# Optimization experiments

Hardware: AMD Instinct MI355X
Metric: run time of the kernel (lower is better)

The kernel has to match this reference:

```python
import jax, jax.numpy as jnp
import numpy as np

SIGMA = 1.0

def setup_inputs() -> dict:
    key = jax.random.key(0)
    k1, k2 = jax.random.split(key)
    z = jax.random.normal(k1, (8192, 1024), dtype=jnp.float32)
    expert_keys = jax.random.normal(k2, (4096, 1024), dtype=jnp.float32)
    return {"z": z, "expert_keys": expert_keys}

def reference(z, expert_keys):
    # squared euclidean distances [N, E] = |z|^2 + |e|^2 - 2 z.e
    z_sq = jnp.sum(z * z, axis=-1, keepdims=True)          # [N, 1]
    e_sq = jnp.sum(expert_keys * expert_keys, axis=-1)     # [E]
    dist2 = z_sq + e_sq[None, :] - 2.0 * (z @ expert_keys.T)
    dist2 = jnp.maximum(dist2, 0.0)
    similarity = jnp.exp(-dist2 / (2.0 * SIGMA ** 2))       # [N, E]
    weights = jax.nn.softmax(similarity, axis=-1)            # [N, E]
    weighted_expert = weights @ expert_keys                  # [N, D]
    return (similarity, weighted_expert)
```

## Files before the change

kernel.cpp:

```cpp
#include <hip/hip_runtime.h>
#include <stdint.h>


#define M_TOK 8192
#define N_EXP 4096
#define D_DIM 1024

typedef __attribute__((ext_vector_type(4))) float f32x4;
typedef __attribute__((ext_vector_type(8))) short short8;
typedef __attribute__((ext_vector_type(4))) unsigned short u16x4;
typedef unsigned short u16;
typedef unsigned int u32;

__device__ __forceinline__ u16 f32_to_bf16(float f) {
  u32 u = __builtin_bit_cast(u32, f);
  u += 0x7fff + ((u >> 16) & 1);
  return (u16)(u >> 16);
}

__device__ __forceinline__ void async16(const void* g, void* l) {
  __builtin_amdgcn_global_load_lds((__attribute__((address_space(1))) void*)(g),
                                   (__attribute__((address_space(3))) void*)(l),
                                   16, 0, 0);
}

__global__ __launch_bounds__(256) void prep_convert2(const float* __restrict__ zsrc,
                                                     const float* __restrict__ esrc,
                                                     u16* __restrict__ zdst,
                                                     u16* __restrict__ edst,
                                                     float* __restrict__ zsq,
                                                     float* __restrict__ esq) {
  int row = blockIdx.x;
  const float* src;
  u16* dst;
  float* sq;
  if (row < M_TOK) {
    src = zsrc + (size_t)row * D_DIM;
    dst = zdst + (size_t)row * D_DIM;
    sq = zsq + row;
  } else {
    int r = row - M_TOK;
    src = esrc + (size_t)r * D_DIM;
    dst = edst + (size_t)r * D_DIM;
    sq = esq + r;
  }
  int t = threadIdx.x;
  const float4 v = ((const float4*)src)[t];
  ushort4 h;
  h.x = f32_to_bf16(v.x); h.y = f32_to_bf16(v.y);
  h.z = f32_to_bf16(v.z); h.w = f32_to_bf16(v.w);
  ((ushort4*)dst)[t] = h;
  float p = v.x * v.x + v.y * v.y + v.z * v.z + v.w * v.w;
#pragma unroll
  for (int off = 1; off < 64; off <<= 1) p += __shfl_xor(p, off, 64);
  __shared__ float partial[4];
  if ((t & 63) == 0) partial[t >> 6] = p;
  __syncthreads();
  if (t == 0) *sq = partial[0] + partial[1] + partial[2] + partial[3];
}

__global__ __launch_bounds__(256) void transpose_bf16(const u16* __restrict__ src,
                                                      u16* __restrict__ dst) {
  __shared__ u16 tile[64][65];
  int e0 = blockIdx.x * 64;
  int d0 = blockIdx.y * 64;
  int t = threadIdx.x;
  int lr = t >> 4;
  int lc = (t & 15) * 4;
#pragma unroll
  for (int r8 = 0; r8 < 4; ++r8) {
    int row = lr + r8 * 16;
    ushort4 v = *(const ushort4*)(src + (size_t)(e0 + row) * D_DIM + d0 + lc);
    tile[row][lc + 0] = v.x; tile[row][lc + 1] = v.y;
    tile[row][lc + 2] = v.z; tile[row][lc + 3] = v.w;
  }
  __syncthreads();
#pragma unroll
  for (int r8 = 0; r8 < 4; ++r8) {
    int dl = lr + r8 * 16;
    ushort4 v;
    v.x = tile[lc + 0][dl]; v.y = tile[lc + 1][dl];
    v.z = tile[lc + 2][dl]; v.w = tile[lc + 3][dl];
    *(ushort4*)(dst + (size_t)(d0 + dl) * N_EXP + e0 + lc) = v;
  }
}

template <int EPI>
__global__ __launch_bounds__(512, 4) void gemm_bt(const u16* __restrict__ A,
                                                  const u16* __restrict__ Bt,
                                                  int Mdim, int Ndim, int Kdim,
                                                  float* __restrict__ out, int ldo,
                                                  const float* __restrict__ a_sq,
                                                  const float* __restrict__ b_sq,
                                                  float* __restrict__ rowsum,
                                                  u16* __restrict__ wb,
                                                  const float* __restrict__ scale) {
  constexpr int BM = 128, BN = 128, BK = 64;
  __shared__ __align__(16) u16 smA[2 * BM * BK];
  __shared__ __align__(16) u16 smB[2 * BN * BK];

  const int nTilesN = Ndim / BN;
  const int nwg = (Mdim / BM) * nTilesN;
  const int cpx = nwg >> 3;
  const int wg = blockIdx.x;
  const int swz = (wg & 7) * cpx + (wg >> 3);
  const int m0 = (swz / nTilesN) * BM;
  const int n0 = (swz % nTilesN) * BN;

  const int t = threadIdx.x;
  const int l = t & 63;
  const int w = t >> 6;
  const int wr = w >> 2;
  const int wc = w & 3;
  const int lr8 = l >> 3;
  const int cswz = (((l & 7) ^ lr8) << 3);
  const int s0 = w * 2, s1 = w * 2 + 1;
  const int str0 = s0 * 8 + lr8, str1 = s1 * 8 + lr8;

  f32x4 acc[4][2];
#pragma unroll
  for (int i = 0; i < 4; ++i)
#pragma unroll
    for (int j = 0; j < 2; ++j) acc[i][j] = (f32x4){0.f, 0.f, 0.f, 0.f};

  const int nIter = Kdim / BK;
  async16(A + (size_t)(m0 + str0) * Kdim + cswz, smA + s0 * 512);
  async16(A + (size_t)(m0 + str1) * Kdim + cswz, smA + s1 * 512);
  async16(Bt + (size_t)(n0 + str0) * Kdim + cswz, smB + s0 * 512);
  async16(Bt + (size_t)(n0 + str1) * Kdim + cswz, smB + s1 * 512);
  __syncthreads();

  int cur = 0;
  for (int it = 0; it < nIter; ++it) {
    if (it + 1 < nIter) {
      const int k0 = (it + 1) * BK;
      const int nb = (cur ^ 1) * 8192;
      async16(A + (size_t)(m0 + str0) * Kdim + k0 + cswz, smA + nb + s0 * 512);
      async16(A + (size_t)(m0 + str1) * Kdim + k0 + cswz, smA + nb + s1 * 512);
      async16(Bt + (size_t)(n0 + str0) * Kdim + k0 + cswz, smB + nb + s0 * 512);
      async16(Bt + (size_t)(n0 + str1) * Kdim + k0 + cswz, smB + nb + s1 * 512);
    }
    const int cbase = cur * 8192;
#pragma unroll
    for (int ks = 0; ks < 2; ++ks) {
      short8 af[4], bf[2];
      const int lrow = l & 15;
      const int kb = ks * 64 + ((l >> 4) << 4);
#pragma unroll
      for (int mi = 0; mi < 4; ++mi) {
        int row = wr * 64 + mi * 16 + lrow;
        int addr = row * 128 + (kb ^ ((row & 7) << 4));
        af[mi] = *(const short8*)(smA + cbase + (addr >> 1));
      }
#pragma unroll
      for (int ni = 0; ni < 2; ++ni) {
        int row = wc * 32 + ni * 16 + lrow;
        int addr = row * 128 + (kb ^ ((row & 7) << 4));
        bf[ni] = *(const short8*)(smB + cbase + (addr >> 1));
      }
#pragma unroll
      for (int mi = 0; mi < 4; ++mi)
#pragma unroll
        for (int ni = 0; ni < 2; ++ni)
          acc[mi][ni] = __builtin_amdgcn_mfma_f32_16x16x32_bf16(
              bf[ni], af[mi], acc[mi][ni], 0, 0, 0);
    }
    __syncthreads();
    cur ^= 1;
  }

  const int lcol = l & 15;
  const int rgrp = l >> 4;
  if (EPI == 1) {
    float* ldsT = ((float*)smA) + w * (16 * 36);
    const int rr = l >> 3;
    const int c4 = (l & 7) * 4;
#pragma unroll
    for (int mi = 0; mi < 4; ++mi) {
      int grow = m0 + wr * 64 + mi * 16 + lcol;
      float zq = a_sq[grow];
#pragma unroll
      for (int ni = 0; ni < 2; ++ni) {
        int ncol = n0 + wc * 32 + ni * 16 + rgrp * 4;
        f32x4 eqv = *(const f32x4*)(b_sq + ncol);
        f32x4 simv;
#pragma unroll
        for (int r = 0; r < 4; ++r) {
          float dist2 = fmaxf(zq + eqv[r] - 2.0f * acc[mi][ni][r], 0.0f);
          simv[r] = __expf(-0.5f * dist2);
        }
        *(f32x4*)(ldsT + lcol * 36 + ni * 16 + rgrp * 4) = simv;
      }
      asm volatile("s_waitcnt lgkmcnt(0)" ::: "memory");
#pragma unroll
      for (int pass = 0; pass < 2; ++pass) {
        int rrow = pass * 8 + rr;
        f32x4 sv = *(const f32x4*)(ldsT + rrow * 36 + c4);
        int growr = m0 + wr * 64 + mi * 16 + rrow;
        size_t gbase = (size_t)growr * ldo + (n0 + wc * 32 + c4);
        __builtin_nontemporal_store(sv, (f32x4*)(out + gbase));
        f32x4 es;
#pragma unroll
        for (int r = 0; r < 4; ++r) es[r] = __expf(sv[r]);
        if (wb) {
          u16x4 wv;
          wv.x = f32_to_bf16(es[0]); wv.y = f32_to_bf16(es[1]);
          wv.z = f32_to_bf16(es[2]); wv.w = f32_to_bf16(es[3]);
          *(u16x4*)(wb + gbase) = wv;
        }
        float p = es[0] + es[1] + es[2] + es[3];
        p += __shfl_xor(p, 1, 64);
        p += __shfl_xor(p, 2, 64);
        p += __shfl_xor(p, 4, 64);
        if ((l & 7) == 0) atomicAdd(&rowsum[growr], p);
      }
    }
  } else {
#pragma unroll
    for (int mi = 0; mi < 4; ++mi) {
      int grow = m0 + wr * 64 + mi * 16 + lcol;
      float s = scale ? (1.0f / scale[grow]) : 1.0f;
#pragma unroll
      for (int ni = 0; ni < 2; ++ni) {
        int ncol = n0 + wc * 32 + ni * 16 + rgrp * 4;
        f32x4 v = acc[mi][ni] * s;
        *(f32x4*)(out + (size_t)grow * ldo + ncol) = v;
      }
    }
  }
}

__global__ __launch_bounds__(256) void weights_kernel(const float* __restrict__ sim,
                                                      const float* __restrict__ rowsum,
                                                      u16* __restrict__ wb) {
  size_t i = ((size_t)blockIdx.x * 256 + threadIdx.x) * 8;
  int row = (int)(i >> 12);
  float inv = 1.0f / rowsum[row];
  float4 a = *(const float4*)(sim + i);
  float4 b = *(const float4*)(sim + i + 4);
  u32 w0 = (u32)f32_to_bf16(__expf(a.x) * inv) | ((u32)f32_to_bf16(__expf(a.y) * inv) << 16);
  u32 w1 = (u32)f32_to_bf16(__expf(a.z) * inv) | ((u32)f32_to_bf16(__expf(a.w) * inv) << 16);
  u32 w2 = (u32)f32_to_bf16(__expf(b.x) * inv) | ((u32)f32_to_bf16(__expf(b.y) * inv) << 16);
  u32 w3 = (u32)f32_to_bf16(__expf(b.z) * inv) | ((u32)f32_to_bf16(__expf(b.w) * inv) << 16);
  uint4 o; o.x = w0; o.y = w1; o.z = w2; o.w = w3;
  *(uint4*)(wb + i) = o;
}

extern "C" void kernel_launch(void* const* d_in, const int* in_sizes, int n_in,
                              void* d_out, int out_size, void* d_ws, size_t ws_size,
                              hipStream_t stream) {
  const float* z = (const float*)d_in[0];
  const float* e = (const float*)d_in[1];
  float* out = (float*)d_out;
  float* sim = out;
  float* wout = out + (size_t)M_TOK * N_EXP;

  char* ws = (char*)d_ws;
  const size_t MB = (size_t)1 << 20;
  const bool fused = ws_size >= 96 * MB + 80 * 1024;

  if (fused) {
    u16* zb  = (u16*)ws;
    u16* eb  = (u16*)(ws + 16 * MB);
    u16* ebT = (u16*)(ws + 24 * MB);
    u16* Wb  = (u16*)(ws + 32 * MB);
    float* z_sq   = (float*)(ws + 96 * MB);
    float* e_sq   = (float*)(ws + 96 * MB + 32768);
    float* rowsum = (float*)(ws + 96 * MB + 49152);

    prep_convert2<<<M_TOK + N_EXP, 256, 0, stream>>>(z, e, zb, eb, z_sq, e_sq);
    transpose_bf16<<<dim3(N_EXP / 64, D_DIM / 64), 256, 0, stream>>>(eb, ebT);
    (void)hipMemsetAsync(rowsum, 0, M_TOK * sizeof(float), stream);

    gemm_bt<1><<<(M_TOK / 128) * (N_EXP / 128), 512, 0, stream>>>(
        zb, eb, M_TOK, N_EXP, D_DIM, sim, N_EXP, z_sq, e_sq, rowsum, Wb, nullptr);

    gemm_bt<0><<<(M_TOK / 128) * (D_DIM / 128), 512, 0, stream>>>(
        Wb, ebT, M_TOK, D_DIM, N_EXP, wout, D_DIM, nullptr, nullptr, nullptr,
        nullptr, rowsum);
  } else {
    u16* Wb  = (u16*)ws;
    u16* zb  = (u16*)ws;
    u16* eb  = (u16*)(ws + 64 * MB);
    u16* ebT = (u16*)(ws + 72 * MB);
    float* z_sq   = (float*)(ws + 80 * MB);
    float* e_sq   = (float*)(ws + 80 * MB + 32768);
    float* rowsum = (float*)(ws + 80 * MB + 49152);

    prep_convert2<<<M_TOK + N_EXP, 256, 0, stream>>>(z, e, zb, eb, z_sq, e_sq);
    transpose_bf16<<<dim3(N_EXP / 64, D_DIM / 64), 256, 0, stream>>>(eb, ebT);
    (void)hipMemsetAsync(rowsum, 0, M_TOK * sizeof(float), stream);

    gemm_bt<1><<<(M_TOK / 128) * (N_EXP / 128), 512, 0, stream>>>(
        zb, eb, M_TOK, N_EXP, D_DIM, sim, N_EXP, z_sq, e_sq, rowsum, nullptr, nullptr);

    weights_kernel<<<(M_TOK * (size_t)N_EXP) / (8 * 256), 256, 0, stream>>>(sim, rowsum, Wb);

    gemm_bt<0><<<(M_TOK / 128) * (D_DIM / 128), 512, 0, stream>>>(
        Wb, ebT, M_TOK, D_DIM, N_EXP, wout, D_DIM, nullptr, nullptr, nullptr,
        nullptr, nullptr);
  }
}
```

Before: 195.7 us.

## Replace rowsum atomics with per-slot partial sums and a reduction kernel

```diff
diff --git a/kernel.cpp b/kernel.cpp
--- a/kernel.cpp
+++ b/kernel.cpp
@@ -85,6 +85,15 @@
   }
 }
 
+__global__ __launch_bounds__(256) void rowsum_reduce(const float* __restrict__ part,
+                                                     float* __restrict__ rowsum) {
+  int r = blockIdx.x * 256 + threadIdx.x;
+  float s = 0.f;
+#pragma unroll 8
+  for (int j = 0; j < 128; ++j) s += part[(size_t)j * M_TOK + r];
+  rowsum[r] = s;
+}
+
 template <int EPI>
 __global__ __launch_bounds__(512, 4) void gemm_bt(const u16* __restrict__ A,
                                                   const u16* __restrict__ Bt,
@@ -92,20 +101,32 @@
                                                   float* __restrict__ out, int ldo,
                                                   const float* __restrict__ a_sq,
                                                   const float* __restrict__ b_sq,
-                                                  float* __restrict__ rowsum,
+                                                  float* __restrict__ rs_part,
                                                   u16* __restrict__ wb,
                                                   const float* __restrict__ scale) {
   constexpr int BM = 128, BN = 128, BK = 64;
   __shared__ __align__(16) u16 smA[2 * BM * BK];
   __shared__ __align__(16) u16 smB[2 * BN * BK];
 
-  const int nTilesN = Ndim / BN;
-  const int nwg = (Mdim / BM) * nTilesN;
-  const int cpx = nwg >> 3;
   const int wg = blockIdx.x;
-  const int swz = (wg & 7) * cpx + (wg >> 3);
-  const int m0 = (swz / nTilesN) * BM;
-  const int n0 = (swz % nTilesN) * BN;
+  int m0, n0, ntile = 0;
+  if (EPI == 1) {
+    const int xcd = wg & 7;
+    const int idx = wg >> 3;
+    const int sup = idx >> 5;
+    const int mloc = (idx & 31) >> 2;
+    const int nloc = idx & 3;
+    m0 = (xcd * 8 + mloc) * BM;
+    ntile = sup * 4 + nloc;
+    n0 = ntile * BN;
+  } else {
+    const int nTilesN = Ndim / BN;
+    const int nwg = (Mdim / BM) * nTilesN;
+    const int cpx = nwg >> 3;
+    const int swz = (wg & 7) * cpx + (wg >> 3);
+    m0 = (swz / nTilesN) * BM;
+    n0 = (swz % nTilesN) * BN;
+  }
 
   const int t = threadIdx.x;
   const int l = t & 63;
@@ -175,6 +196,7 @@
     float* ldsT = ((float*)smA) + w * (16 * 36);
     const int rr = l >> 3;
     const int c4 = (l & 7) * 4;
+    const int slot = ntile * 4 + wc;
 #pragma unroll
     for (int mi = 0; mi < 4; ++mi) {
       int grow = m0 + wr * 64 + mi * 16 + lcol;
@@ -212,7 +234,7 @@
         p += __shfl_xor(p, 1, 64);
         p += __shfl_xor(p, 2, 64);
         p += __shfl_xor(p, 4, 64);
-        if ((l & 7) == 0) atomicAdd(&rowsum[growr], p);
+        if ((l & 7) == 0) rs_part[(size_t)slot * M_TOK + growr] = p;
       }
     }
   } else {
@@ -257,23 +279,25 @@
 
   char* ws = (char*)d_ws;
   const size_t MB = (size_t)1 << 20;
-  const bool fused = ws_size >= 96 * MB + 80 * 1024;
+  const bool fused = ws_size >= 100 * MB + 96 * 1024;
 
   if (fused) {
     u16* zb  = (u16*)ws;
     u16* eb  = (u16*)(ws + 16 * MB);
     u16* ebT = (u16*)(ws + 24 * MB);
     u16* Wb  = (u16*)(ws + 32 * MB);
-    float* z_sq   = (float*)(ws + 96 * MB);
-    float* e_sq   = (float*)(ws + 96 * MB + 32768);
-    float* rowsum = (float*)(ws + 96 * MB + 49152);
+    float* rs_part = (float*)(ws + 96 * MB);
+    float* z_sq   = (float*)(ws + 100 * MB);
+    float* e_sq   = (float*)(ws + 100 * MB + 32768);
+    float* rowsum = (float*)(ws + 100 * MB + 49152);
 
     prep_convert2<<<M_TOK + N_EXP, 256, 0, stream>>>(z, e, zb, eb, z_sq, e_sq);
     transpose_bf16<<<dim3(N_EXP / 64, D_DIM / 64), 256, 0, stream>>>(eb, ebT);
-    (void)hipMemsetAsync(rowsum, 0, M_TOK * sizeof(float), stream);
 
     gemm_bt<1><<<(M_TOK / 128) * (N_EXP / 128), 512, 0, stream>>>(
-        zb, eb, M_TOK, N_EXP, D_DIM, sim, N_EXP, z_sq, e_sq, rowsum, Wb, nullptr);
+        zb, eb, M_TOK, N_EXP, D_DIM, sim, N_EXP, z_sq, e_sq, rs_part, Wb, nullptr);
+
+    rowsum_reduce<<<M_TOK / 256, 256, 0, stream>>>(rs_part, rowsum);
 
     gemm_bt<0><<<(M_TOK / 128) * (D_DIM / 128), 512, 0, stream>>>(
         Wb, ebT, M_TOK, D_DIM, N_EXP, wout, D_DIM, nullptr, nullptr, nullptr,
@@ -283,16 +307,18 @@
     u16* zb  = (u16*)ws;
     u16* eb  = (u16*)(ws + 64 * MB);
     u16* ebT = (u16*)(ws + 72 * MB);
-    float* z_sq   = (float*)(ws + 80 * MB);
-    float* e_sq   = (float*)(ws + 80 * MB + 32768);
-    float* rowsum = (float*)(ws + 80 * MB + 49152);
+    float* rs_part = (float*)(ws + 80 * MB);
+    float* z_sq   = (float*)(ws + 84 * MB);
+    float* e_sq   = (float*)(ws + 84 * MB + 32768);
+    float* rowsum = (float*)(ws + 84 * MB + 49152);
 
     prep_convert2<<<M_TOK + N_EXP, 256, 0, stream>>>(z, e, zb, eb, z_sq, e_sq);
     transpose_bf16<<<dim3(N_EXP / 64, D_DIM / 64), 256, 0, stream>>>(eb, ebT);
-    (void)hipMemsetAsync(rowsum, 0, M_TOK * sizeof(float), stream);
 
     gemm_bt<1><<<(M_TOK / 128) * (N_EXP / 128), 512, 0, stream>>>(
-        zb, eb, M_TOK, N_EXP, D_DIM, sim, N_EXP, z_sq, e_sq, rowsum, nullptr, nullptr);
+        zb, eb, M_TOK, N_EXP, D_DIM, sim, N_EXP, z_sq, e_sq, rs_part, nullptr, nullptr);
+
+    rowsum_reduce<<<M_TOK / 256, 256, 0, stream>>>(rs_part, rowsum);
 
     weights_kernel<<<(M_TOK * (size_t)N_EXP) / (8 * 256), 256, 0, stream>>>(sim, rowsum, Wb);
 
```

Result: faster. 187.9 us (-4.0%).
